# Optimization experiments

Measured on AMD Instinct MI355X. Metric: run time of the kernel, lower is better.

The kernel has to match this reference:

```python
import jax, jax.numpy as jnp
import numpy as np

AGENT, WIN, DIM, HEADS = 6, 7, 256, 8


def _relative_position_index():
    # Exactly mirrors the torch buffer construction (meshgrid indexing='ij').
    coords = np.stack(np.meshgrid(np.arange(AGENT), np.arange(WIN), np.arange(WIN), indexing='ij'))
    cf = coords.reshape(3, -1)  # (3, N)
    rel = cf[:, :, None] - cf[:, None, :]  # (3, N, N)
    rel = np.transpose(rel, (1, 2, 0)).copy()  # (N, N, 3)
    rel[..., 0] += AGENT - 1
    rel[..., 1] += WIN - 1
    rel[..., 2] += WIN - 1
    rel[..., 0] *= (2 * WIN - 1) * (2 * WIN - 1)
    rel[..., 1] *= 2 * WIN - 1
    return rel.sum(-1).astype(np.int32)  # (N, N)


def setup_inputs() -> dict:
    key = jax.random.key(0)
    k1, k2, k3, k4 = jax.random.split(key, 4)
    b, X, Y = 1, 16, 16
    table_size = (2 * AGENT - 1) * (2 * WIN - 1) * (2 * WIN - 1)  # 1859
    x = jax.random.normal(k1, (b, AGENT, X, Y, WIN, WIN, DIM), dtype=jnp.float32)
    w_qkv = jax.random.normal(k2, (DIM, 3 * DIM), dtype=jnp.float32) * 0.02
    w_out = jax.random.normal(k3, (DIM, DIM), dtype=jnp.float32) * 0.02
    bias_table = jax.random.normal(k4, (table_size, HEADS), dtype=jnp.float32) * 0.02
    rel_index = jnp.asarray(_relative_position_index())
    return {"x": x, "w_qkv": w_qkv, "w_out": w_out, "bias_table": bias_table, "rel_index": rel_index}


def reference(x, w_qkv, w_out, bias_table, rel_index):
    b, L, X, Y, W1, W2, D = x.shape
    h = bias_table.shape[-1]
    dh = D // h
    scale = dh ** -0.5
    N = L * W1 * W2
    B = b * X * Y
    # 'b l x y w1 w2 d -> (b x y) (l w1 w2) d'
    xw = jnp.transpose(x, (0, 2, 3, 1, 4, 5, 6)).reshape(B, N, D)
    qkv = xw @ w_qkv  # (B, N, 3D)
    q, k, v = jnp.split(qkv, 3, axis=-1)
    def heads(t):
        return jnp.transpose(t.reshape(B, N, h, dh), (0, 2, 1, 3))  # (B, h, N, dh)
    q, k, v = heads(q) * scale, heads(k), heads(v)
    sim = jnp.einsum('bhid,bhjd->bhij', q, k)  # (B, h, N, N)
    bias = bias_table[rel_index]  # (N, N, h)
    sim = sim + jnp.transpose(bias, (2, 0, 1))[None]
    attn = jax.nn.softmax(sim, axis=-1)
    out = jnp.einsum('bhij,bhjd->bhid', attn, v)  # (B, h, N, dh)
    out = jnp.transpose(out, (0, 2, 1, 3)).reshape(B, N, h * dh)
    out = out @ w_out  # (B, N, D)
    out = out.reshape(b, X, Y, L, W1, W2, D)
    return jnp.transpose(out, (0, 3, 1, 2, 4, 5, 6))  # (b, l, x, y, w1, w2, d)
```

## Files before the change

kernel.cpp:

```cpp
#include <hip/hip_runtime.h>
#include <hip/hip_bf16.h>

#define NTOK 294
#define NB   256
#define NN   (NTOK*NTOK)
#define ROWS_M (NB*NTOK)
#define USN  19267584ULL

typedef __bf16 bf16x8 __attribute__((ext_vector_type(8)));
typedef float  f32x4  __attribute__((ext_vector_type(4)));
typedef unsigned short ushort_t;

union Bf8 { bf16x8 v; unsigned short u[8]; };

__device__ inline unsigned short f2bf(float f) {
    unsigned int u = __float_as_uint(f);
    return (unsigned short)((u + 0x7FFFu + ((u >> 16) & 1u)) >> 16);
}

__device__ inline bf16x8 cvt8(float4 a, float4 b) {
    bf16x8 r;
    r[0] = (__bf16)a.x; r[1] = (__bf16)a.y; r[2] = (__bf16)a.z; r[3] = (__bf16)a.w;
    r[4] = (__bf16)b.x; r[5] = (__bf16)b.y; r[6] = (__bf16)b.z; r[7] = (__bf16)b.w;
    return r;
}

__global__ void bias_expand(const float* __restrict__ table,
                            const int* __restrict__ rel,
                            float* __restrict__ biasQ) {
    int t = blockIdx.x * 256 + threadIdx.x;
    if (t >= NN) return;
    int idx = rel[t];
    const float* src = table + idx * 8;
#pragma unroll
    for (int h = 0; h < 8; ++h)
        biasQ[h * NN + t] = src[h];
}

__global__ void wt_prep(const float* __restrict__ wqkv,
                        const float* __restrict__ wout,
                        ushort_t* __restrict__ wqkvT,
                        ushort_t* __restrict__ woutT) {
    int t = blockIdx.x * 256 + threadIdx.x;
    if (t < 768 * 256) {
        int n = t >> 8, k = t & 255;
        wqkvT[t] = f2bf(wqkv[k * 768 + n]);
    } else {
        int u = t - 768 * 256;
        int n = u >> 8, k = u & 255;
        woutT[u] = f2bf(wout[k * 256 + n]);
    }
}

__global__ __launch_bounds__(256) void qkv_gemm_mfma2(const float* __restrict__ x,
                                                      const ushort_t* __restrict__ wqkvT,
                                                      ushort_t* __restrict__ qb,
                                                      ushort_t* __restrict__ kb,
                                                      ushort_t* __restrict__ vt) {
    const int t    = threadIdx.x;
    const int lane = t & 63;
    const int w    = t >> 6;
    const int wm   = w >> 1, wn = w & 1;
    const int l15  = lane & 15, kg8 = (lane >> 4) * 8;
    const int cb   = blockIdx.x * 128;
    const int mt   = blockIdx.y * 128;

    const float* arow[4];
#pragma unroll
    for (int fi = 0; fi < 4; ++fi) {
        int m  = mt + wm * 64 + fi * 16 + l15;
        int Bi = m / NTOK, n = m - Bi * NTOK;
        int l  = n / 49,   ww = n - l * 49;
        int xx = Bi >> 4,  yy = Bi & 15;
        arow[fi] = x + (size_t)((((l * 16 + xx) * 16 + yy) * 49 + ww) << 8) + kg8;
    }
    const ushort_t* brow[4];
#pragma unroll
    for (int fj = 0; fj < 4; ++fj) {
        int nn = cb + wn * 64 + fj * 16 + l15;
        brow[fj] = wqkvT + (size_t)nn * 256 + kg8;
    }

    f32x4 acc[4][4];
#pragma unroll
    for (int i = 0; i < 4; ++i)
#pragma unroll
        for (int j = 0; j < 4; ++j) acc[i][j] = (f32x4){0.f, 0.f, 0.f, 0.f};

#pragma unroll 2
    for (int kk = 0; kk < 256; kk += 32) {
        bf16x8 af[4], bfr[4];
#pragma unroll
        for (int fi = 0; fi < 4; ++fi) {
            float4 f0 = *(const float4*)(arow[fi] + kk);
            float4 f1 = *(const float4*)(arow[fi] + kk + 4);
            af[fi] = cvt8(f0, f1);
        }
#pragma unroll
        for (int fj = 0; fj < 4; ++fj)
            bfr[fj] = *(const bf16x8*)(brow[fj] + kk);
#pragma unroll
        for (int fi = 0; fi < 4; ++fi)
#pragma unroll
            for (int fj = 0; fj < 4; ++fj)
                acc[fi][fj] = __builtin_amdgcn_mfma_f32_16x16x32_bf16(
                    af[fi], bfr[fj], acc[fi][fj], 0, 0, 0);
    }

    const float scale = 0.17677669529663687f;
    const int rq   = lane >> 4;
    const int cidx = lane & 15;
#pragma unroll
    for (int fi = 0; fi < 4; ++fi) {
#pragma unroll
        for (int reg = 0; reg < 4; ++reg) {
            int mm  = mt + wm * 64 + fi * 16 + rq * 4 + reg;
            int Bi2 = mm / NTOK, n2 = mm - Bi2 * NTOK;
#pragma unroll
            for (int fj = 0; fj < 4; ++fj) {
                int c     = cb + wn * 64 + fj * 16 + cidx;
                int which = c >> 8;
                int rr    = c & 255;
                int hh    = rr >> 5, di = rr & 31;
                int bhi   = Bi2 * 8 + hh;
                if (which == 0) {
                    qb[((size_t)bhi * NTOK + n2) * 32 + di] = f2bf(acc[fi][fj][reg] * scale);
                } else if (which == 1) {
                    kb[((size_t)bhi * NTOK + n2) * 32 + di] = f2bf(acc[fi][fj][reg]);
                } else {
                    vt[((size_t)bhi * 32 + di) * NTOK + n2] = f2bf(acc[fi][fj][reg]);
                }
            }
        }
    }
}

#define S_KS 40
#define S_VS 328
#define S_PS 40
__global__ __launch_bounds__(256) void attn_mfma(ushort_t* __restrict__ qb,
                                                 const ushort_t* __restrict__ kb,
                                                 const ushort_t* __restrict__ vt,
                                                 const float* __restrict__ biasQ) {
    __shared__ ushort_t ks[320 * S_KS];
    __shared__ ushort_t vs[32 * S_VS];
    __shared__ ushort_t ps[4 * 16 * S_PS];
    const int qt = blockIdx.x, bh = blockIdx.y, h = bh & 7;
    const int tid = threadIdx.x;

    const unsigned int* ksrc = (const unsigned int*)(kb + (size_t)bh * NTOK * 32);
    for (int t = tid; t < 294 * 16; t += 256) {
        int r = t >> 4, i = t & 15;
        *(unsigned int*)&ks[r * S_KS + 2 * i] = ksrc[t];
    }
    for (int t = tid; t < 26 * 16; t += 256) {
        int r = 294 + (t >> 4), i = t & 15;
        *(unsigned int*)&ks[r * S_KS + 2 * i] = 0u;
    }
    const unsigned int* vsrc = (const unsigned int*)(vt + (size_t)bh * 32 * NTOK);
    for (int t = tid; t < 32 * 147; t += 256) {
        int d = t / 147, i = t - d * 147;
        *(unsigned int*)&vs[d * S_VS + 2 * i] = vsrc[t];
    }
    for (int t = tid; t < 32 * 17; t += 256) {
        int d = t / 17, i = 147 + (t - d * 17);
        *(unsigned int*)&vs[d * S_VS + 2 * i] = 0u;
    }
    __syncthreads();

    const int wave = tid >> 6, lane = tid & 63;
    const int c = lane & 15, g = lane >> 4;
    const int q0 = qt * 128 + wave * 32;

    bf16x8 qf[2];
#pragma unroll
    for (int qs = 0; qs < 2; ++qs) {
        int qa = q0 + qs * 16 + c; if (qa > 293) qa = 293;
        qf[qs] = *(const bf16x8*)&qb[((size_t)bh * NTOK + qa) * 32 + 8 * g];
    }
    f32x4 acc_o[2][2];
    float psum[2][4];
#pragma unroll
    for (int qs = 0; qs < 2; ++qs) {
#pragma unroll
        for (int hf = 0; hf < 2; ++hf) acc_o[qs][hf] = (f32x4){0.f, 0.f, 0.f, 0.f};
#pragma unroll
        for (int rg = 0; rg < 4; ++rg) psum[qs][rg] = 0.f;
    }
    ushort_t* pw = ps + wave * 16 * S_PS;
    const float* bbase = biasQ + (size_t)h * NN;

    for (int kt = 0; kt < 10; ++kt) {
        const int kbase = kt * 32;
        bf16x8 kf[2], vf[2];
#pragma unroll
        for (int ksub = 0; ksub < 2; ++ksub)
            kf[ksub] = *(const bf16x8*)&ks[(kbase + ksub * 16 + c) * S_KS + 8 * g];
#pragma unroll
        for (int hf = 0; hf < 2; ++hf)
            vf[hf] = *(const bf16x8*)&vs[(hf * 16 + c) * S_VS + kbase + 8 * g];

#pragma unroll
        for (int qs = 0; qs < 2; ++qs) {
            f32x4 s0 = __builtin_amdgcn_mfma_f32_16x16x32_bf16(
                qf[qs], kf[0], (f32x4){0.f, 0.f, 0.f, 0.f}, 0, 0, 0);
            f32x4 s1 = __builtin_amdgcn_mfma_f32_16x16x32_bf16(
                qf[qs], kf[1], (f32x4){0.f, 0.f, 0.f, 0.f}, 0, 0, 0);
            const int qrb = q0 + qs * 16 + g * 4;
#pragma unroll
            for (int rg = 0; rg < 4; ++rg) {
                int qa = qrb + rg; if (qa > 293) qa = 293;
                const float* bp = bbase + (size_t)qa * NTOK;
#pragma unroll
                for (int ksub = 0; ksub < 2; ++ksub) {
                    int ka = kbase + ksub * 16 + c;
                    int kc = ka > 293 ? 293 : ka;
                    float bias = (ka < NTOK) ? bp[kc] : -1e4f;
                    float s = (ksub ? s1[rg] : s0[rg]) + bias;
                    float p = __expf(s);
                    psum[qs][rg] += p;
                    pw[(g * 4 + rg) * S_PS + ksub * 16 + c] = f2bf(p);
                }
            }
            bf16x8 pa = *(const bf16x8*)&pw[c * S_PS + 8 * g];
#pragma unroll
            for (int hf = 0; hf < 2; ++hf)
                acc_o[qs][hf] = __builtin_amdgcn_mfma_f32_16x16x32_bf16(
                    pa, vf[hf], acc_o[qs][hf], 0, 0, 0);
        }
    }

#pragma unroll
    for (int qs = 0; qs < 2; ++qs)
#pragma unroll
        for (int rg = 0; rg < 4; ++rg) {
            float v = psum[qs][rg];
            v += __shfl_xor(v, 1); v += __shfl_xor(v, 2);
            v += __shfl_xor(v, 4); v += __shfl_xor(v, 8);
            psum[qs][rg] = 1.0f / v;
        }

#pragma unroll
    for (int qs = 0; qs < 2; ++qs) {
        const int qrb = q0 + qs * 16 + g * 4;
#pragma unroll
        for (int rg = 0; rg < 4; ++rg) {
            int qa = qrb + rg;
            if (qa < NTOK) {
#pragma unroll
                for (int hf = 0; hf < 2; ++hf) {
                    float val = acc_o[qs][hf][rg] * psum[qs][rg];
                    qb[((size_t)bh * NTOK + qa) * 32 + hf * 16 + c] = f2bf(val);
                }
            }
        }
    }
}

__global__ __launch_bounds__(256) void out_gemm_mfma2(const ushort_t* __restrict__ ob,
                                                      const ushort_t* __restrict__ woutT,
                                                      float* __restrict__ out) {
    const int t    = threadIdx.x;
    const int lane = t & 63;
    const int w    = t >> 6;
    const int wm   = w >> 1, wn = w & 1;
    const int l15  = lane & 15, kg8 = (lane >> 4) * 8;
    const int cb   = blockIdx.x * 128;
    const int mt   = blockIdx.y * 128;

    const ushort_t* abase[4];
#pragma unroll
    for (int fi = 0; fi < 4; ++fi) {
        int m  = mt + wm * 64 + fi * 16 + l15;
        int Bi = m / NTOK, n = m - Bi * NTOK;
        abase[fi] = ob + ((size_t)(Bi * 8) * NTOK + n) * 32 + kg8;
    }
    const ushort_t* brow[4];
#pragma unroll
    for (int fj = 0; fj < 4; ++fj) {
        int nn = cb + wn * 64 + fj * 16 + l15;
        brow[fj] = woutT + (size_t)nn * 256 + kg8;
    }

    f32x4 acc[4][4];
#pragma unroll
    for (int i = 0; i < 4; ++i)
#pragma unroll
        for (int j = 0; j < 4; ++j) acc[i][j] = (f32x4){0.f, 0.f, 0.f, 0.f};

#pragma unroll 2
    for (int kk = 0; kk < 256; kk += 32) {
        const int hstep = kk >> 5;
        bf16x8 af[4], bfr[4];
#pragma unroll
        for (int fi = 0; fi < 4; ++fi)
            af[fi] = *(const bf16x8*)(abase[fi] + (size_t)hstep * NTOK * 32);
#pragma unroll
        for (int fj = 0; fj < 4; ++fj)
            bfr[fj] = *(const bf16x8*)(brow[fj] + kk);
#pragma unroll
        for (int fi = 0; fi < 4; ++fi)
#pragma unroll
            for (int fj = 0; fj < 4; ++fj)
                acc[fi][fj] = __builtin_amdgcn_mfma_f32_16x16x32_bf16(
                    af[fi], bfr[fj], acc[fi][fj], 0, 0, 0);
    }

    const int rq   = lane >> 4;
    const int cidx = lane & 15;
#pragma unroll
    for (int fi = 0; fi < 4; ++fi) {
#pragma unroll
        for (int reg = 0; reg < 4; ++reg) {
            int mm  = mt + wm * 64 + fi * 16 + rq * 4 + reg;
            int Bi2 = mm / NTOK, n2 = mm - Bi2 * NTOK;
            int l2  = n2 / 49,   w2 = n2 - l2 * 49;
            int xx2 = Bi2 >> 4,  yy2 = Bi2 & 15;
            float* orow = out + (size_t)((((l2 * 16 + xx2) * 16 + yy2) * 49 + w2) << 8);
#pragma unroll
            for (int fj = 0; fj < 4; ++fj) {
                int c = cb + wn * 64 + fj * 16 + cidx;
                orow[c] = acc[fi][fj][reg];
            }
        }
    }
}

extern "C" void kernel_launch(void* const* d_in, const int* in_sizes, int n_in,
                              void* d_out, int out_size, void* d_ws, size_t ws_size,
                              hipStream_t stream) {
    const float* x     = (const float*)d_in[0];
    const float* wqkv  = (const float*)d_in[1];
    const float* wout  = (const float*)d_in[2];
    const float* table = (const float*)d_in[3];
    const int*   rel   = (const int*)d_in[4];
    float* out = (float*)d_out;

    ushort_t* qb    = (ushort_t*)d_ws;
    ushort_t* kb    = qb + USN;
    ushort_t* vt    = kb + USN;
    float*    biasQ = (float*)(vt + USN);
    ushort_t* wqkvT = (ushort_t*)(biasQ + 8 * NN);
    ushort_t* woutT = wqkvT + 768 * 256;

    hipLaunchKernelGGL(bias_expand, dim3((NN + 255) / 256), dim3(256), 0, stream,
                       table, rel, biasQ);
    hipLaunchKernelGGL(wt_prep, dim3((768 * 256 + 256 * 256) / 256), dim3(256), 0, stream,
                       wqkv, wout, wqkvT, woutT);
    hipLaunchKernelGGL(qkv_gemm_mfma2, dim3(6, 588), dim3(256), 0, stream,
                       x, wqkvT, qb, kb, vt);
    hipLaunchKernelGGL(attn_mfma, dim3(3, 2048), dim3(256), 0, stream,
                       qb, kb, vt, biasQ);
    hipLaunchKernelGGL(out_gemm_mfma2, dim3(2, 588), dim3(256), 0, stream,
                       qb, woutT, out);
}
```

Baseline: 489.2 us.

## Stage converted x tile in LDS once and loop over all QKV column tiles

The QKV GEMM now loads each 128-row block of fp32 x once, converts it to bf16, and stores it in a 64KB XOR-swizzled shared buffer. One workgroup then loops over all six 128-column output tiles, so the 2D grid of 6x588 becomes 588 blocks. Before, every column tile reread x from global memory and redid the fp32-to-bf16 conversion, so x was read six times. The trade-off is lower parallelism and occupancy from 64KB of LDS per block and fewer blocks, and the per-tile work inside each block is now serialised.

Result: faster. 474.7 us (-2.9%).

```diff
diff --git a/kernel.cpp b/kernel.cpp
--- a/kernel.cpp
+++ b/kernel.cpp
@@ -52,83 +52,99 @@
     }
 }
 
-__global__ __launch_bounds__(256) void qkv_gemm_mfma2(const float* __restrict__ x,
+__global__ __launch_bounds__(256) void qkv_gemm_mfma3(const float* __restrict__ x,
                                                       const ushort_t* __restrict__ wqkvT,
                                                       ushort_t* __restrict__ qb,
                                                       ushort_t* __restrict__ kb,
                                                       ushort_t* __restrict__ vt) {
+    __shared__ ushort_t As[128 * 256];
     const int t    = threadIdx.x;
     const int lane = t & 63;
     const int w    = t >> 6;
     const int wm   = w >> 1, wn = w & 1;
     const int l15  = lane & 15, kg8 = (lane >> 4) * 8;
-    const int cb   = blockIdx.x * 128;
-    const int mt   = blockIdx.y * 128;
-
-    const float* arow[4];
-#pragma unroll
-    for (int fi = 0; fi < 4; ++fi) {
-        int m  = mt + wm * 64 + fi * 16 + l15;
+    const int mt   = blockIdx.x * 128;
+
+    {
+        const int r  = t >> 1;
+        const int h2 = t & 1;
+        int m  = mt + r;
         int Bi = m / NTOK, n = m - Bi * NTOK;
         int l  = n / 49,   ww = n - l * 49;
         int xx = Bi >> 4,  yy = Bi & 15;
-        arow[fi] = x + (size_t)((((l * 16 + xx) * 16 + yy) * 49 + ww) << 8) + kg8;
-    }
-    const ushort_t* brow[4];
-#pragma unroll
-    for (int fj = 0; fj < 4; ++fj) {
-        int nn = cb + wn * 64 + fj * 16 + l15;
-        brow[fj] = wqkvT + (size_t)nn * 256 + kg8;
-    }
-
-    f32x4 acc[4][4];
-#pragma unroll
-    for (int i = 0; i < 4; ++i)
-#pragma unroll
-        for (int j = 0; j < 4; ++j) acc[i][j] = (f32x4){0.f, 0.f, 0.f, 0.f};
-
-#pragma unroll 2
-    for (int kk = 0; kk < 256; kk += 32) {
-        bf16x8 af[4], bfr[4];
-#pragma unroll
-        for (int fi = 0; fi < 4; ++fi) {
-            float4 f0 = *(const float4*)(arow[fi] + kk);
-            float4 f1 = *(const float4*)(arow[fi] + kk + 4);
-            af[fi] = cvt8(f0, f1);
-        }
-#pragma unroll
-        for (int fj = 0; fj < 4; ++fj)
-            bfr[fj] = *(const bf16x8*)(brow[fj] + kk);
-#pragma unroll
-        for (int fi = 0; fi < 4; ++fi)
-#pragma unroll
-            for (int fj = 0; fj < 4; ++fj)
-                acc[fi][fj] = __builtin_amdgcn_mfma_f32_16x16x32_bf16(
-                    af[fi], bfr[fj], acc[fi][fj], 0, 0, 0);
-    }
+        const float* arow = x + (size_t)((((l * 16 + xx) * 16 + yy) * 49 + ww) << 8) + h2 * 32;
+#pragma unroll
+        for (int kk = 0; kk < 256; kk += 64) {
+#pragma unroll
+            for (int c = 0; c < 4; ++c) {
+                float4 f0 = *(const float4*)(arow + kk + c * 8);
+                float4 f1 = *(const float4*)(arow + kk + c * 8 + 4);
+                int idx = (r * 256 + kk + h2 * 32 + c * 8) ^ ((r & 7) << 3);
+                *(bf16x8*)&As[idx] = cvt8(f0, f1);
+            }
+        }
+    }
+    __syncthreads();
 
     const float scale = 0.17677669529663687f;
     const int rq   = lane >> 4;
     const int cidx = lane & 15;
-#pragma unroll
-    for (int fi = 0; fi < 4; ++fi) {
-#pragma unroll
-        for (int reg = 0; reg < 4; ++reg) {
-            int mm  = mt + wm * 64 + fi * 16 + rq * 4 + reg;
-            int Bi2 = mm / NTOK, n2 = mm - Bi2 * NTOK;
-#pragma unroll
-            for (int fj = 0; fj < 4; ++fj) {
-                int c     = cb + wn * 64 + fj * 16 + cidx;
-                int which = c >> 8;
-                int rr    = c & 255;
-                int hh    = rr >> 5, di = rr & 31;
-                int bhi   = Bi2 * 8 + hh;
-                if (which == 0) {
-                    qb[((size_t)bhi * NTOK + n2) * 32 + di] = f2bf(acc[fi][fj][reg] * scale);
-                } else if (which == 1) {
-                    kb[((size_t)bhi * NTOK + n2) * 32 + di] = f2bf(acc[fi][fj][reg]);
-                } else {
-                    vt[((size_t)bhi * 32 + di) * NTOK + n2] = f2bf(acc[fi][fj][reg]);
+
+    for (int ct = 0; ct < 6; ++ct) {
+        const int cb = ct * 128;
+        const ushort_t* brow[4];
+#pragma unroll
+        for (int fj = 0; fj < 4; ++fj) {
+            int nn = cb + wn * 64 + fj * 16 + l15;
+            brow[fj] = wqkvT + (size_t)nn * 256 + kg8;
+        }
+
+        f32x4 acc[4][4];
+#pragma unroll
+        for (int i = 0; i < 4; ++i)
+#pragma unroll
+            for (int j = 0; j < 4; ++j) acc[i][j] = (f32x4){0.f, 0.f, 0.f, 0.f};
+
+#pragma unroll 2
+        for (int kk = 0; kk < 256; kk += 32) {
+            bf16x8 af[4], bfr[4];
+#pragma unroll
+            for (int fi = 0; fi < 4; ++fi) {
+                int rr  = wm * 64 + fi * 16 + l15;
+                int idx = (rr * 256 + kk + kg8) ^ ((rr & 7) << 3);
+                af[fi] = *(const bf16x8*)&As[idx];
+            }
+#pragma unroll
+            for (int fj = 0; fj < 4; ++fj)
+                bfr[fj] = *(const bf16x8*)(brow[fj] + kk);
+#pragma unroll
+            for (int fi = 0; fi < 4; ++fi)
+#pragma unroll
+                for (int fj = 0; fj < 4; ++fj)
+                    acc[fi][fj] = __builtin_amdgcn_mfma_f32_16x16x32_bf16(
+                        af[fi], bfr[fj], acc[fi][fj], 0, 0, 0);
+        }
+
+#pragma unroll
+        for (int fi = 0; fi < 4; ++fi) {
+#pragma unroll
+            for (int reg = 0; reg < 4; ++reg) {
+                int mm  = mt + wm * 64 + fi * 16 + rq * 4 + reg;
+                int Bi2 = mm / NTOK, n2 = mm - Bi2 * NTOK;
+#pragma unroll
+                for (int fj = 0; fj < 4; ++fj) {
+                    int c     = cb + wn * 64 + fj * 16 + cidx;
+                    int which = c >> 8;
+                    int rr    = c & 255;
+                    int hh    = rr >> 5, di = rr & 31;
+                    int bhi   = Bi2 * 8 + hh;
+                    if (which == 0) {
+                        qb[((size_t)bhi * NTOK + n2) * 32 + di] = f2bf(acc[fi][fj][reg] * scale);
+                    } else if (which == 1) {
+                        kb[((size_t)bhi * NTOK + n2) * 32 + di] = f2bf(acc[fi][fj][reg]);
+                    } else {
+                        vt[((size_t)bhi * 32 + di) * NTOK + n2] = f2bf(acc[fi][fj][reg]);
+                    }
                 }
             }
         }
@@ -347,7 +363,7 @@
                        table, rel, biasQ);
     hipLaunchKernelGGL(wt_prep, dim3((768 * 256 + 256 * 256) / 256), dim3(256), 0, stream,
                        wqkv, wout, wqkvT, woutT);
-    hipLaunchKernelGGL(qkv_gemm_mfma2, dim3(6, 588), dim3(256), 0, stream,
+    hipLaunchKernelGGL(qkv_gemm_mfma3, dim3(588), dim3(256), 0, stream,
                        x, wqkvT, qb, kb, vt);
     hipLaunchKernelGGL(attn_mfma, dim3(3, 2048), dim3(256), 0, stream,
                        qb, kb, vt, biasQ);
```

## Pre-convert x to bf16, store V row-major, swap GEMM grid order

Applied to the files above, without the earlier changes.

A new kernel converts x from fp32 to bf16 once, so the QKV GEMM reads bf16 operands directly instead of loading fp32 and converting in the inner loop. V is now written in the same row-major layout as Q and K, which avoids the strided transposed stores, and the attention kernel transposes V into shared memory with byte permutes. The GEMM grids are reordered so the M tile runs along blockIdx.x, which changes how consecutive blocks reuse data in cache. The cost is an extra pass over x plus a workspace buffer the size of x in bf16.

Measured after the change: 441.5 us. -9.7%, faster.

```diff
diff --git a/kernel.cpp b/kernel.cpp
--- a/kernel.cpp
+++ b/kernel.cpp
@@ -10,8 +10,6 @@
 typedef __bf16 bf16x8 __attribute__((ext_vector_type(8)));
 typedef float  f32x4  __attribute__((ext_vector_type(4)));
 typedef unsigned short ushort_t;
-
-union Bf8 { bf16x8 v; unsigned short u[8]; };
 
 __device__ inline unsigned short f2bf(float f) {
     unsigned int u = __float_as_uint(f);
@@ -52,27 +50,37 @@
     }
 }
 
-__global__ __launch_bounds__(256) void qkv_gemm_mfma2(const float* __restrict__ x,
+__global__ void x_cvt(const float* __restrict__ x, ushort_t* __restrict__ xb) {
+    const size_t total = USN / 8;
+    size_t stride = (size_t)gridDim.x * 256;
+    for (size_t i = blockIdx.x * 256 + threadIdx.x; i < total; i += stride) {
+        float4 f0 = ((const float4*)x)[2 * i];
+        float4 f1 = ((const float4*)x)[2 * i + 1];
+        ((bf16x8*)xb)[i] = cvt8(f0, f1);
+    }
+}
+
+__global__ __launch_bounds__(256) void qkv_gemm_mfma4(const ushort_t* __restrict__ xb,
                                                       const ushort_t* __restrict__ wqkvT,
                                                       ushort_t* __restrict__ qb,
                                                       ushort_t* __restrict__ kb,
-                                                      ushort_t* __restrict__ vt) {
+                                                      ushort_t* __restrict__ vb) {
     const int t    = threadIdx.x;
     const int lane = t & 63;
     const int w    = t >> 6;
     const int wm   = w >> 1, wn = w & 1;
     const int l15  = lane & 15, kg8 = (lane >> 4) * 8;
-    const int cb   = blockIdx.x * 128;
-    const int mt   = blockIdx.y * 128;
-
-    const float* arow[4];
+    const int mt   = blockIdx.x * 128;
+    const int cb   = blockIdx.y * 128;
+
+    const ushort_t* arow[4];
 #pragma unroll
     for (int fi = 0; fi < 4; ++fi) {
         int m  = mt + wm * 64 + fi * 16 + l15;
         int Bi = m / NTOK, n = m - Bi * NTOK;
         int l  = n / 49,   ww = n - l * 49;
         int xx = Bi >> 4,  yy = Bi & 15;
-        arow[fi] = x + (size_t)((((l * 16 + xx) * 16 + yy) * 49 + ww) << 8) + kg8;
+        arow[fi] = xb + ((size_t)((((l * 16 + xx) * 16 + yy) * 49 + ww)) << 8) + kg8;
     }
     const ushort_t* brow[4];
 #pragma unroll
@@ -91,11 +99,8 @@
     for (int kk = 0; kk < 256; kk += 32) {
         bf16x8 af[4], bfr[4];
 #pragma unroll
-        for (int fi = 0; fi < 4; ++fi) {
-            float4 f0 = *(const float4*)(arow[fi] + kk);
-            float4 f1 = *(const float4*)(arow[fi] + kk + 4);
-            af[fi] = cvt8(f0, f1);
-        }
+        for (int fi = 0; fi < 4; ++fi)
+            af[fi] = *(const bf16x8*)(arow[fi] + kk);
 #pragma unroll
         for (int fj = 0; fj < 4; ++fj)
             bfr[fj] = *(const bf16x8*)(brow[fj] + kk);
@@ -123,13 +128,9 @@
                 int rr    = c & 255;
                 int hh    = rr >> 5, di = rr & 31;
                 int bhi   = Bi2 * 8 + hh;
-                if (which == 0) {
-                    qb[((size_t)bhi * NTOK + n2) * 32 + di] = f2bf(acc[fi][fj][reg] * scale);
-                } else if (which == 1) {
-                    kb[((size_t)bhi * NTOK + n2) * 32 + di] = f2bf(acc[fi][fj][reg]);
-                } else {
-                    vt[((size_t)bhi * 32 + di) * NTOK + n2] = f2bf(acc[fi][fj][reg]);
-                }
+                ushort_t* dst = which == 0 ? qb : (which == 1 ? kb : vb);
+                float vvv = acc[fi][fj][reg] * (which == 0 ? scale : 1.0f);
+                dst[((size_t)bhi * NTOK + n2) * 32 + di] = f2bf(vvv);
             }
         }
     }
@@ -140,7 +141,7 @@
 #define S_PS 40
 __global__ __launch_bounds__(256) void attn_mfma(ushort_t* __restrict__ qb,
                                                  const ushort_t* __restrict__ kb,
-                                                 const ushort_t* __restrict__ vt,
+                                                 const ushort_t* __restrict__ vb,
                                                  const float* __restrict__ biasQ) {
     __shared__ ushort_t ks[320 * S_KS];
     __shared__ ushort_t vs[32 * S_VS];
@@ -157,10 +158,14 @@
         int r = 294 + (t >> 4), i = t & 15;
         *(unsigned int*)&ks[r * S_KS + 2 * i] = 0u;
     }
-    const unsigned int* vsrc = (const unsigned int*)(vt + (size_t)bh * 32 * NTOK);
-    for (int t = tid; t < 32 * 147; t += 256) {
-        int d = t / 147, i = t - d * 147;
-        *(unsigned int*)&vs[d * S_VS + 2 * i] = vsrc[t];
+    const unsigned int* vsrc = (const unsigned int*)(vb + (size_t)bh * NTOK * 32);
+    for (int t = tid; t < 147 * 16; t += 256) {
+        int r2 = t >> 4;
+        int i  = t & 15;
+        unsigned int A = vsrc[(2 * r2) * 16 + i];
+        unsigned int B = vsrc[(2 * r2 + 1) * 16 + i];
+        *(unsigned int*)&vs[(2 * i) * S_VS + 2 * r2]     = __byte_perm(A, B, 0x5410);
+        *(unsigned int*)&vs[(2 * i + 1) * S_VS + 2 * r2] = __byte_perm(A, B, 0x7632);
     }
     for (int t = tid; t < 32 * 17; t += 256) {
         int d = t / 17, i = 147 + (t - d * 17);
@@ -265,8 +270,8 @@
     const int w    = t >> 6;
     const int wm   = w >> 1, wn = w & 1;
     const int l15  = lane & 15, kg8 = (lane >> 4) * 8;
-    const int cb   = blockIdx.x * 128;
-    const int mt   = blockIdx.y * 128;
+    const int mt   = blockIdx.x * 128;
+    const int cb   = blockIdx.y * 128;
 
     const ushort_t* abase[4];
 #pragma unroll
@@ -338,8 +343,9 @@
 
     ushort_t* qb    = (ushort_t*)d_ws;
     ushort_t* kb    = qb + USN;
-    ushort_t* vt    = kb + USN;
-    float*    biasQ = (float*)(vt + USN);
+    ushort_t* vb    = kb + USN;
+    ushort_t* xb    = vb + USN;
+    float*    biasQ = (float*)(xb + USN);
     ushort_t* wqkvT = (ushort_t*)(biasQ + 8 * NN);
     ushort_t* woutT = wqkvT + 768 * 256;
 
@@ -347,10 +353,11 @@
                        table, rel, biasQ);
     hipLaunchKernelGGL(wt_prep, dim3((768 * 256 + 256 * 256) / 256), dim3(256), 0, stream,
                        wqkv, wout, wqkvT, woutT);
-    hipLaunchKernelGGL(qkv_gemm_mfma2, dim3(6, 588), dim3(256), 0, stream,
-                       x, wqkvT, qb, kb, vt);
+    hipLaunchKernelGGL(x_cvt, dim3(2048), dim3(256), 0, stream, x, xb);
+    hipLaunchKernelGGL(qkv_gemm_mfma4, dim3(588, 6), dim3(256), 0, stream,
+                       xb, wqkvT, qb, kb, vb);
     hipLaunchKernelGGL(attn_mfma, dim3(3, 2048), dim3(256), 0, stream,
-                       qb, kb, vt, biasQ);
-    hipLaunchKernelGGL(out_gemm_mfma2, dim3(2, 588), dim3(256), 0, stream,
+                       qb, kb, vb, biasQ);
+    hipLaunchKernelGGL(out_gemm_mfma2, dim3(588, 2), dim3(256), 0, stream,
                        qb, woutT, out);
 }
```
